# Kernel tuning notes

Measured on AMD Instinct MI355X. Metric: run time of the kernel, lower is better.

## Reference

```python
import jax, jax.numpy as jnp
import numpy as np

NUM_USERS = 100000
NUM_ITEMS = 50000
N_NODES = NUM_USERS + NUM_ITEMS
EMBED_DIM = 64
N_EDGES = 2400000
NUM_LAYERS = 3
DROPOUT_P = 0.2


def setup_inputs() -> dict:
    key = jax.random.key(0)
    k1, k2, k3, k4, k5 = jax.random.split(key, 5)
    # xavier_uniform bound = sqrt(6/(fan_in+fan_out))
    bu = np.sqrt(6.0 / (NUM_USERS + EMBED_DIM)).astype(np.float32)
    bi = np.sqrt(6.0 / (NUM_ITEMS + EMBED_DIM)).astype(np.float32)
    user_emb = jax.random.uniform(k1, (NUM_USERS, EMBED_DIM), jnp.float32, -bu, bu)
    item_emb = jax.random.uniform(k2, (NUM_ITEMS, EMBED_DIM), jnp.float32, -bi, bi)
    adj_rows = jax.random.randint(k3, (N_EDGES,), 0, N_NODES, dtype=jnp.int32)
    adj_cols = jax.random.randint(k4, (N_EDGES,), 0, N_NODES, dtype=jnp.int32)
    # normalized adjacency values (positive, small) mimicking D^-1/2 A D^-1/2
    adj_vals = jax.random.uniform(k5, (N_EDGES,), jnp.float32, 0.0, 0.25)
    return {"user_emb": user_emb, "item_emb": item_emb,
            "adj_rows": adj_rows, "adj_cols": adj_cols, "adj_vals": adj_vals}


def _spmm(rows, cols, vals, x):
    # y[r] += vals[e] * x[cols[e]] for each edge e with rows[e]==r
    gathered = x[cols] * vals[:, None]          # [E, D]
    return jax.ops.segment_sum(gathered, rows, num_segments=N_NODES)


def reference(user_emb, item_emb, adj_rows, adj_cols, adj_vals):
    x = jnp.concatenate([user_emb, item_emb], axis=0)          # [N, D]
    # dropout (training=True), fixed key for determinism
    keep = jax.random.bernoulli(jax.random.key(42), 1.0 - DROPOUT_P, x.shape)
    x = jnp.where(keep, x / (1.0 - DROPOUT_P), 0.0)
    acc = x  # running sum over layer embeddings (== mean * (L+1))
    for _ in range(NUM_LAYERS):
        x = _spmm(adj_rows, adj_cols, adj_vals, x)
        acc = acc + x
    final = acc / jnp.float32(NUM_LAYERS + 1)
    return final[:NUM_USERS], final[NUM_USERS:]
```

## Files before the change

kernel.cpp:

```cpp
#include <hip/hip_runtime.h>


static constexpr int NU = 100000;
static constexpr int NI = 50000;
static constexpr int NN = NU + NI;
static constexpr int D  = 64;
static constexpr int E  = 2400000;
static constexpr int XN = NN * D;
static constexpr int XH = XN / 2;
static constexpr int NB = (NN + 1023) >> 10;
static constexpr int BPC = 24000;
static constexpr int BIN_T = 256;
static constexpr int BIN_U = 16;
static constexpr int BIN_CHUNK = BIN_T * BIN_U;
static constexpr int BGRID = (E + BIN_CHUNK - 1) / BIN_CHUNK;
static constexpr int DGRID = (XH + 255) / 256;

typedef _Float16 half_t;
typedef _Float16 half8 __attribute__((ext_vector_type(8)));

__device__ __forceinline__ unsigned rotl32(unsigned x, int r) {
    return (x << r) | (x >> (32 - r));
}

__device__ __forceinline__ void threefry2x32(unsigned k0, unsigned k1,
                                             unsigned x0, unsigned x1,
                                             unsigned& o0, unsigned& o1) {
    unsigned ks2 = k0 ^ k1 ^ 0x1BD11BDAu;
    x0 += k0; x1 += k1;
#define TF_R(r) { x0 += x1; x1 = rotl32(x1, r); x1 ^= x0; }
    TF_R(13) TF_R(15) TF_R(26) TF_R(6)   x0 += k1;  x1 += ks2 + 1u;
    TF_R(17) TF_R(29) TF_R(16) TF_R(24)  x0 += ks2; x1 += k0 + 2u;
    TF_R(13) TF_R(15) TF_R(26) TF_R(6)   x0 += k0;  x1 += k1 + 3u;
    TF_R(17) TF_R(29) TF_R(16) TF_R(24)  x0 += k1;  x1 += ks2 + 4u;
    TF_R(13) TF_R(15) TF_R(26) TF_R(6)   x0 += ks2; x1 += k0 + 5u;
#undef TF_R
    o0 = x0; o1 = x1;
}

__device__ __forceinline__ float dropout_val(const float* __restrict__ ue,
                                             const float* __restrict__ ie,
                                             int i, unsigned bits) {
    float src = (i < NU * D) ? ue[i] : ie[i - NU * D];
    float u = __uint_as_float((bits >> 9) | 0x3f800000u) - 1.0f;
    return (u < 0.8f) ? (src / 0.8f) : 0.0f;
}

__global__ void __launch_bounds__(BIN_T) k_pre(const int* __restrict__ rows,
                                               const int* __restrict__ cols,
                                               const float* __restrict__ vals,
                                               int2* __restrict__ stg,
                                               int* __restrict__ pcnt,
                                               const float* __restrict__ ue,
                                               const float* __restrict__ ie,
                                               half_t* __restrict__ x0h) {
    __shared__ int lcnt[NB];
    __shared__ int gbase[NB];
    int tid = threadIdx.x;
    if (blockIdx.x >= BGRID) {
        int j = (blockIdx.x - BGRID) * BIN_T + tid;
        if (j >= XH) return;
        unsigned o0, o1, b0, b1;
        threefry2x32(0u, 42u, 0u, (unsigned)j, o0, o1);        b0 = o0 ^ o1;
        threefry2x32(0u, 42u, 0u, (unsigned)(j + XH), o0, o1); b1 = o0 ^ o1;
        x0h[j]      = (half_t)dropout_val(ue, ie, j, b0);
        x0h[j + XH] = (half_t)dropout_val(ue, ie, j + XH, b1);
        return;
    }
    for (int i = tid; i < NB; i += BIN_T) lcnt[i] = 0;
    __syncthreads();
    int base = blockIdx.x * BIN_CHUNK;
    int lp[BIN_U];
    int2 rec[BIN_U];
    #pragma unroll
    for (int u = 0; u < BIN_U; ++u) {
        int idx = base + u * BIN_T + tid;
        if (idx < E) {
            int row = rows[idx];
            int col = cols[idx];
            float v = vals[idx];
            unsigned q = min(__float2int_rn(v * 65536.f), 16383);
            int b = row >> 10;
            int loff = atomicAdd(&lcnt[b], 1);
            lp[u] = (b << 13) | loff;
            rec[u] = make_int2((int)((q << 18) | (unsigned)col), row);
        } else {
            lp[u] = -1;
        }
    }
    __syncthreads();
    for (int i = tid; i < NB; i += BIN_T)
        gbase[i] = atomicAdd(&pcnt[i * 16], lcnt[i]);
    __syncthreads();
    #pragma unroll
    for (int u = 0; u < BIN_U; ++u) {
        if (lp[u] >= 0) {
            int b = lp[u] >> 13;
            int pos = gbase[b] + (lp[u] & 8191);
            if (pos < BPC) stg[(size_t)b * BPC + pos] = rec[u];
        }
    }
}

__global__ void __launch_bounds__(1024) k_bsort(const int2* __restrict__ stg,
                                                const int* __restrict__ pcnt,
                                                int* __restrict__ rp,
                                                unsigned* __restrict__ ev) {
    __shared__ int cnt[1024];
    __shared__ int wsum[16];
    __shared__ int sbb;
    int b = blockIdx.x;
    int t = threadIdx.x;
    cnt[t] = 0;
    if (t < 64) {
        int a = 0;
        for (int i = t; i < b; i += 64) a += pcnt[i * 16];
        #pragma unroll
        for (int d = 1; d < 64; d <<= 1) a += __shfl_xor(a, d);
        if (t == 0) sbb = a;
    }
    if (b == 0 && t == 0) rp[NN] = E;
    __syncthreads();
    int tot = min(pcnt[b * 16], BPC);
    int bb = sbb;
    const int2* s = stg + (size_t)b * BPC;
    for (int i = t; i < tot; i += 1024)
        atomicAdd(&cnt[s[i].y & 1023], 1);
    __syncthreads();
    int v = cnt[t];
    int lane = t & 63, w = t >> 6;
    int x = v;
    #pragma unroll
    for (int d = 1; d < 64; d <<= 1) {
        int y = __shfl_up(x, d);
        if (lane >= d) x += y;
    }
    if (lane == 63) wsum[w] = x;
    __syncthreads();
    if (w == 0 && lane < 16) {
        int sv = wsum[lane];
        #pragma unroll
        for (int d = 1; d < 16; d <<= 1) {
            int y = __shfl_up(sv, d);
            if (lane >= d) sv += y;
        }
        wsum[lane] = sv;
    }
    __syncthreads();
    int excl = ((w > 0) ? wsum[w - 1] : 0) + x - v;
    int row = (b << 10) + t;
    if (row < NN) rp[row] = bb + excl;
    __syncthreads();
    cnt[t] = bb + excl;
    __syncthreads();
    for (int i = t; i < tot; i += 1024) {
        int2 r = s[i];
        int pos = atomicAdd(&cnt[r.y & 1023], 1);
        ev[pos] = (unsigned)r.x;
    }
}

template <int MODE>
__global__ void __launch_bounds__(256) k_spmm(const int* __restrict__ rp,
                                              const unsigned* __restrict__ ev,
                                              const half_t* __restrict__ xh,
                                              half_t* __restrict__ yh,
                                              const half_t* __restrict__ x0h,
                                              const half_t* __restrict__ y1h,
                                              float* __restrict__ out) {
    int wid  = threadIdx.x >> 6;
    int lane = threadIdx.x & 63;
    int g    = lane >> 3;
    int l    = lane & 7;
    int row  = blockIdx.x * 32 + wid * 8 + g;
    if (row >= NN) return;
    const float inv = 1.0f / 65536.0f;
    int s0  = rp[row];
    int cnt = rp[row + 1] - s0;
    float acc[8] = {0.f, 0.f, 0.f, 0.f, 0.f, 0.f, 0.f, 0.f};
    int gl = g << 3;
    int pc0 = (l < cnt)     ? (int)ev[s0 + l] : 0;
    int pc1 = (8 + l < cnt) ? (int)ev[s0 + 8 + l] : 0;
    for (int base = 0; base < cnt; base += 16) {
        int n0 = base + 16 + l;
        int n1 = base + 24 + l;
        int pn0 = (n0 < cnt) ? (int)ev[s0 + n0] : 0;
        int pn1 = (n1 < cnt) ? (int)ev[s0 + n1] : 0;
        int pj[16];
        #pragma unroll
        for (int j = 0; j < 8; ++j) {
            pj[j]     = __shfl(pc0, gl | j);
            pj[8 + j] = __shfl(pc1, gl | j);
        }
        half8 xv[16];
        #pragma unroll
        for (int j = 0; j < 16; ++j)
            xv[j] = *(const half8*)(xh + (pj[j] & 0x3FFFF) * 64 + l * 8);
        #pragma unroll
        for (int j = 0; j < 16; ++j) {
            float vj = (float)((unsigned)pj[j] >> 18) * inv;
            #pragma unroll
            for (int k = 0; k < 8; ++k)
                acc[k] = fmaf(vj, (float)xv[j][k], acc[k]);
        }
        pc0 = pn0;
        pc1 = pn1;
    }
    int o = row * 64 + l * 8;
    if (MODE == 0) {
        half8 st;
        #pragma unroll
        for (int k = 0; k < 8; ++k) st[k] = (half_t)acc[k];
        *(half8*)(yh + o) = st;
    } else {
        const half8 a0 = *(const half8*)(x0h + o);
        const half8 a1 = *(const half8*)(y1h + o);
        const half8 a2 = *(const half8*)(xh + o);
        float r[8];
        #pragma unroll
        for (int k = 0; k < 8; ++k)
            r[k] = ((float)a0[k] + (float)a1[k] + (float)a2[k] + acc[k]) * 0.25f;
        *(float4*)(out + o)     = make_float4(r[0], r[1], r[2], r[3]);
        *(float4*)(out + o + 4) = make_float4(r[4], r[5], r[6], r[7]);
    }
}

extern "C" void kernel_launch(void* const* d_in, const int* in_sizes, int n_in,
                              void* d_out, int out_size, void* d_ws, size_t ws_size,
                              hipStream_t stream) {
    const float* ue   = (const float*)d_in[0];
    const float* ie   = (const float*)d_in[1];
    const int*   rows = (const int*)d_in[2];
    const int*   cols = (const int*)d_in[3];
    const float* vals = (const float*)d_in[4];
    float* out = (float*)d_out;

    half_t*   X0h   = (half_t*)d_ws;
    half_t*   Y1h   = X0h + XN;
    half_t*   Y2h   = Y1h + XN;
    int2*     stg   = (int2*)Y1h;
    unsigned* ev    = (unsigned*)(Y2h + XN);
    int*      rp    = (int*)(ev + E);
    int*      pcnt  = rp + NN + 4;

    (void)hipMemsetAsync(pcnt, 0, NB * 16 * sizeof(int), stream);
    k_pre<<<BGRID + DGRID, BIN_T, 0, stream>>>(rows, cols, vals, stg, pcnt,
                                               ue, ie, X0h);
    k_bsort<<<NB, 1024, 0, stream>>>(stg, pcnt, rp, ev);

    int sgrid = (NN + 31) / 32;
    k_spmm<0><<<sgrid, 256, 0, stream>>>(rp, ev, X0h, Y1h, nullptr, nullptr, nullptr);
    k_spmm<0><<<sgrid, 256, 0, stream>>>(rp, ev, Y1h, Y2h, nullptr, nullptr, nullptr);
    k_spmm<1><<<sgrid, 256, 0, stream>>>(rp, ev, Y2h, nullptr, X0h, Y1h, out);
}
```

Measured before the change: 300.6 us.

## Vectorize preprocessing loads and cache bucket records in registers for sort

The dropout branch now handles 8 contiguous elements per thread, with float4 loads and a half8 store, and multiplies by 1.25 instead of dividing by 0.8. The binning branch loads rows, cols and vals as int4/float4 vectors. The bucket sort reads each staged record once into a 24-entry register array and reuses it for both the counting pass and the scatter pass, instead of reading global memory twice. The trade-offs are higher register pressure, which can lower occupancy, and the assumption that each bucket holds at most 24*1024 records, which BPC=24000 satisfies. Each thread's edges are now contiguous rather than strided, which changes the order of the shared-memory atomics.

```diff
diff --git a/kernel.cpp b/kernel.cpp
--- a/kernel.cpp
+++ b/kernel.cpp
@@ -7,14 +7,15 @@
 static constexpr int D  = 64;
 static constexpr int E  = 2400000;
 static constexpr int XN = NN * D;
-static constexpr int XH = XN / 2;
+static constexpr int NUD = NU * D;
 static constexpr int NB = (NN + 1023) >> 10;
 static constexpr int BPC = 24000;
 static constexpr int BIN_T = 256;
 static constexpr int BIN_U = 16;
 static constexpr int BIN_CHUNK = BIN_T * BIN_U;
 static constexpr int BGRID = (E + BIN_CHUNK - 1) / BIN_CHUNK;
-static constexpr int DGRID = (XH + 255) / 256;
+static constexpr int DGRID = (XN / 8 + BIN_T - 1) / BIN_T;
+static constexpr int RPT = 24;
 
 typedef _Float16 half_t;
 typedef _Float16 half8 __attribute__((ext_vector_type(8)));
@@ -38,14 +39,6 @@
     o0 = x0; o1 = x1;
 }
 
-__device__ __forceinline__ float dropout_val(const float* __restrict__ ue,
-                                             const float* __restrict__ ie,
-                                             int i, unsigned bits) {
-    float src = (i < NU * D) ? ue[i] : ie[i - NU * D];
-    float u = __uint_as_float((bits >> 9) | 0x3f800000u) - 1.0f;
-    return (u < 0.8f) ? (src / 0.8f) : 0.0f;
-}
-
 __global__ void __launch_bounds__(BIN_T) k_pre(const int* __restrict__ rows,
                                                const int* __restrict__ cols,
                                                const float* __restrict__ vals,
@@ -58,13 +51,23 @@
     __shared__ int gbase[NB];
     int tid = threadIdx.x;
     if (blockIdx.x >= BGRID) {
-        int j = (blockIdx.x - BGRID) * BIN_T + tid;
-        if (j >= XH) return;
-        unsigned o0, o1, b0, b1;
-        threefry2x32(0u, 42u, 0u, (unsigned)j, o0, o1);        b0 = o0 ^ o1;
-        threefry2x32(0u, 42u, 0u, (unsigned)(j + XH), o0, o1); b1 = o0 ^ o1;
-        x0h[j]      = (half_t)dropout_val(ue, ie, j, b0);
-        x0h[j + XH] = (half_t)dropout_val(ue, ie, j + XH, b1);
+        int j8 = (blockIdx.x - BGRID) * BIN_T + tid;
+        if (j8 >= XN / 8) return;
+        int j0 = j8 * 8;
+        const float* src = (j0 < NUD) ? (ue + j0) : (ie + (j0 - NUD));
+        float4 f0 = *(const float4*)(src);
+        float4 f1 = *(const float4*)(src + 4);
+        float f[8] = {f0.x, f0.y, f0.z, f0.w, f1.x, f1.y, f1.z, f1.w};
+        half8 st;
+        #pragma unroll
+        for (int k = 0; k < 8; ++k) {
+            unsigned o0, o1;
+            threefry2x32(0u, 42u, 0u, (unsigned)(j0 + k), o0, o1);
+            unsigned bits = o0 ^ o1;
+            float u = __uint_as_float((bits >> 9) | 0x3f800000u) - 1.0f;
+            st[k] = (half_t)((u < 0.8f) ? f[k] * 1.25f : 0.0f);
+        }
+        *(half8*)(x0h + j0) = st;
         return;
     }
     for (int i = tid; i < NB; i += BIN_T) lcnt[i] = 0;
@@ -72,20 +75,35 @@
     int base = blockIdx.x * BIN_CHUNK;
     int lp[BIN_U];
     int2 rec[BIN_U];
-    #pragma unroll
-    for (int u = 0; u < BIN_U; ++u) {
-        int idx = base + u * BIN_T + tid;
-        if (idx < E) {
-            int row = rows[idx];
-            int col = cols[idx];
-            float v = vals[idx];
-            unsigned q = min(__float2int_rn(v * 65536.f), 16383);
-            int b = row >> 10;
-            int loff = atomicAdd(&lcnt[b], 1);
-            lp[u] = (b << 13) | loff;
-            rec[u] = make_int2((int)((q << 18) | (unsigned)col), row);
-        } else {
-            lp[u] = -1;
+    int4  r4[4], c4[4];
+    float4 v4[4];
+    #pragma unroll
+    for (int u4 = 0; u4 < 4; ++u4) {
+        int e0 = base + (u4 * BIN_T + tid) * 4;
+        if (e0 < E) {
+            r4[u4] = *(const int4*)(rows + e0);
+            c4[u4] = *(const int4*)(cols + e0);
+            v4[u4] = *(const float4*)(vals + e0);
+        }
+    }
+    #pragma unroll
+    for (int u4 = 0; u4 < 4; ++u4) {
+        int e0 = base + (u4 * BIN_T + tid) * 4;
+        int rr[4] = {r4[u4].x, r4[u4].y, r4[u4].z, r4[u4].w};
+        int cc[4] = {c4[u4].x, c4[u4].y, c4[u4].z, c4[u4].w};
+        float vv[4] = {v4[u4].x, v4[u4].y, v4[u4].z, v4[u4].w};
+        #pragma unroll
+        for (int k = 0; k < 4; ++k) {
+            int u = u4 * 4 + k;
+            if (e0 < E) {
+                unsigned q = min(__float2int_rn(vv[k] * 65536.f), 16383);
+                int b = rr[k] >> 10;
+                int loff = atomicAdd(&lcnt[b], 1);
+                lp[u] = (b << 13) | loff;
+                rec[u] = make_int2((int)((q << 18) | (unsigned)cc[k]), rr[k]);
+            } else {
+                lp[u] = -1;
+            }
         }
     }
     __syncthreads();
@@ -124,8 +142,17 @@
     int tot = min(pcnt[b * 16], BPC);
     int bb = sbb;
     const int2* s = stg + (size_t)b * BPC;
-    for (int i = t; i < tot; i += 1024)
-        atomicAdd(&cnt[s[i].y & 1023], 1);
+    int2 rec[RPT];
+    #pragma unroll
+    for (int u = 0; u < RPT; ++u) {
+        int i = t + u * 1024;
+        if (i < tot) rec[u] = s[i];
+    }
+    #pragma unroll
+    for (int u = 0; u < RPT; ++u) {
+        int i = t + u * 1024;
+        if (i < tot) atomicAdd(&cnt[rec[u].y & 1023], 1);
+    }
     __syncthreads();
     int v = cnt[t];
     int lane = t & 63, w = t >> 6;
@@ -153,10 +180,13 @@
     __syncthreads();
     cnt[t] = bb + excl;
     __syncthreads();
-    for (int i = t; i < tot; i += 1024) {
-        int2 r = s[i];
-        int pos = atomicAdd(&cnt[r.y & 1023], 1);
-        ev[pos] = (unsigned)r.x;
+    #pragma unroll
+    for (int u = 0; u < RPT; ++u) {
+        int i = t + u * 1024;
+        if (i < tot) {
+            int pos = atomicAdd(&cnt[rec[u].y & 1023], 1);
+            ev[pos] = (unsigned)rec[u].x;
+        }
     }
 }
 
```

Measured after the change: 290.4 us. 1.03x faster.
